# Performance work log

Hardware: AMD Instinct MI355X
Metric: run time of the kernel (lower is better)

The kernel has to match this reference:

```python
import jax, jax.numpy as jnp
import numpy as np

H = 224  # config.output_height
W = 224  # config.output_width
N = 381  # config.num_frequency_bins (one splat per bin)
B = 16   # frames rendered per batch


def setup_inputs() -> dict:
    key = jax.random.key(0)
    k1, k2, k3 = jax.random.split(key, 3)
    # positions in [-0.9, 0.9] (spiral stays inside the frame)
    positions = jax.random.uniform(k1, (B, N, 2), dtype=jnp.float32, minval=-0.9, maxval=0.9)
    colors = jax.random.uniform(k2, (B, N, 3), dtype=jnp.float32)  # RGB in [0,1]
    # sizes in pixels, matching base_size=2 + size_scale=8*softplus(...)
    sizes = jax.random.uniform(k3, (B, N), dtype=jnp.float32, minval=2.0, maxval=10.0)
    return {"positions": positions, "colors": colors, "sizes": sizes}


def reference(positions, colors, sizes):
    """Soft (differentiable) rasterization of Gaussian point splats.

    positions: [B,N,2] in [-1,1]; colors: [B,N,3] in [0,1]; sizes: [B,N] pixels.
    Returns image [B,H,W,3] in [0,1].
    """
    gy = jnp.linspace(-1.0, 1.0, H, dtype=positions.dtype)
    gx = jnp.linspace(-1.0, 1.0, W, dtype=positions.dtype)
    # squared distance from every pixel to every point: [B,N,H,W]
    dx = gx[None, None, None, :] - positions[:, :, 0, None, None]
    dy = gy[None, None, :, None] - positions[:, :, 1, None, None]
    d2 = dx * dx + dy * dy
    # pixel size -> normalized coords ([-1,1] spans H pixels)
    sigma = sizes * (2.0 / H)  # [B,N]
    inv_two_var = 1.0 / (2.0 * sigma * sigma + 1e-8)
    weights = jnp.exp(-d2 * inv_two_var[:, :, None, None])  # [B,N,H,W]
    image = jnp.einsum('bnhw,bnc->bhwc', weights, colors)   # accumulate splats
    return jnp.clip(image, 0.0, 1.0)
```

## Files before the change

### kernel.cpp

```cpp
#include <hip/hip_runtime.h>
#include <math.h>

#define HH 224
#define WW 224
#define NS 381
#define BB 16
#define TPB 256
#define TILE_W 32
#define TILE_H 32
#define TILES_X (WW / TILE_W)
#define BLKS_PER_IMG (TILES_X * (HH / TILE_H))
#define NBLK (BB * BLKS_PER_IMG)
#define NS_PAD 384
#define CUT 19.93f
#define CH 32
#define EY_STRIDE 33
#define EXT_STRIDE 40
#define MT_STRIDE 40
#define OUT_STRIDE 97

typedef _Float16 f16x8 __attribute__((ext_vector_type(8)));
typedef _Float16 f16x2 __attribute__((ext_vector_type(2)));
typedef float    f32x4 __attribute__((ext_vector_type(4)));

union SharedU {
    struct {
        float    ey[CH * EY_STRIDE];
        _Float16 ext[TILE_W * EXT_STRIDE];
        _Float16 mt[96 * MT_STRIDE];
    } s;
    float outb[TILE_W * OUT_STRIDE];
};

__global__ __launch_bounds__(TPB) void splat_render(const float* __restrict__ pos,
                                                    const float* __restrict__ col,
                                                    const float* __restrict__ siz,
                                                    float* __restrict__ out) {
    __shared__ float4 geo[NS_PAD];
    __shared__ int cnt;
    __shared__ SharedU u;

    int blk = blockIdx.x;
    int b = blk / BLKS_PER_IMG;
    int t = blk - b * BLKS_PER_IMG;
    int tile_y = t / TILES_X;
    int tile_x = t - tile_y * TILES_X;

    if (threadIdx.x == 0) cnt = 0;
    __syncthreads();

    const float gstep = 2.0f / (float)(WW - 1);
    float x0 = -1.0f + (float)(tile_x * TILE_W) * gstep;
    float x1 = x0 + (float)(TILE_W - 1) * gstep;
    float y0 = -1.0f + (float)(tile_y * TILE_H) * gstep;
    float y1 = y0 + (float)(TILE_H - 1) * gstep;

    const float2* pb = (const float2*)(pos + (size_t)b * NS * 2);
    const float*  cb = col + (size_t)b * NS * 3;
    const float*  sb = siz + (size_t)b * NS;
    int lane = threadIdx.x & 63;
    int wave = threadIdx.x >> 6;

    for (int r = 0; r < 2; ++r) {
        int i = threadIdx.x + r * TPB;
        bool pass = false;
        float4 A = make_float4(0.f, 0.f, 0.f, 0.f);
        if (i < NS) {
            float2 p = pb[i];
            float sg = sb[i] * (2.0f / (float)HH);
            float itv = 1.0f / (2.0f * sg * sg + 1e-8f);
            float ss = sqrtf(itv * 1.44269504088896340736f);
            float u_ = p.x * ss, v_ = p.y * ss;
            float dxm = fmaxf(fmaxf(x0 * ss - u_, u_ - x1 * ss), 0.0f);
            float dym = fmaxf(fmaxf(y0 * ss - v_, v_ - y1 * ss), 0.0f);
            pass = fmaf(dxm, dxm, dym * dym) < CUT;
            if (pass) {
                unsigned pr = (unsigned)fmaf(cb[3 * i + 0], 1023.0f, 0.5f);
                unsigned pg = (unsigned)fmaf(cb[3 * i + 1], 1023.0f, 0.5f);
                unsigned pc = (unsigned)fmaf(cb[3 * i + 2], 1023.0f, 0.5f);
                A = make_float4(ss, -u_, -v_, __uint_as_float(pr | (pg << 10) | (pc << 20)));
            }
        }
        unsigned long long mask = __ballot(pass);
        int ofs = __popcll(mask & ((1ull << lane) - 1ull));
        int tot = __popcll(mask);
        int base = 0;
        if (lane == 0 && tot) base = atomicAdd(&cnt, tot);
        base = __shfl(base, 0);
        if (pass) geo[base + ofs] = A;
    }
    __syncthreads();
    int m = cnt;
    int m_pad = (m + (CH - 1)) & ~(CH - 1);
    for (int i = m + threadIdx.x; i < m_pad; i += TPB)
        geo[i] = make_float4(0.f, 0.f, 0.f, 0.f);
    __syncthreads();

    int ct = wave & 1;
    int qbase = (wave >> 1) * 48;
    f32x4 acc0 = {0.f, 0.f, 0.f, 0.f};
    f32x4 acc1 = {0.f, 0.f, 0.f, 0.f};
    f32x4 acc2 = {0.f, 0.f, 0.f, 0.f};

    int p2  = threadIdx.x & 15;
    int rEy = threadIdx.x & 31;
    float gyr = y0 + (float)rEy * gstep;

    for (int nb = 0; nb < m_pad; nb += CH) {
#pragma unroll
        for (int k = 0; k < 4; ++k) {
            int n = (threadIdx.x >> 5) + 8 * k;
            float4 A = geo[nb + n];
            float dy = fmaf(gyr, A.x, A.z);
            u.s.ey[n * EY_STRIDE + rEy] = __builtin_amdgcn_exp2f(-dy * dy);
        }
        __syncthreads();
        float4 A0 = geo[nb + 2 * p2];
        float4 A1 = geo[nb + 2 * p2 + 1];
#pragma unroll
        for (int k = 0; k < 2; ++k) {
            int c = (threadIdx.x >> 4) + 16 * k;
            float gxc = x0 + (float)c * gstep;
            float dx0 = fmaf(gxc, A0.x, A0.y);
            float dx1 = fmaf(gxc, A1.x, A1.y);
            f16x2 h;
            h.x = (_Float16)__builtin_amdgcn_exp2f(-dx0 * dx0);
            h.y = (_Float16)__builtin_amdgcn_exp2f(-dx1 * dx1);
            *(f16x2*)&u.s.ext[c * EXT_STRIDE + 2 * p2] = h;
        }
        unsigned pk0 = __float_as_uint(A0.w), pk1 = __float_as_uint(A1.w);
#pragma unroll
        for (int k = 0; k < 6; ++k) {
            int q = (threadIdx.x >> 4) + 16 * k;
            int r = (q * 21846) >> 16;
            int chn = q - 3 * r;
            float cf0 = (float)((pk0 >> (10 * chn)) & 1023u) * (1.0f / 1023.0f);
            float cf1 = (float)((pk1 >> (10 * chn)) & 1023u) * (1.0f / 1023.0f);
            f16x2 h;
            h.x = (_Float16)(u.s.ey[(2 * p2) * EY_STRIDE + r] * cf0);
            h.y = (_Float16)(u.s.ey[(2 * p2 + 1) * EY_STRIDE + r] * cf1);
            *(f16x2*)&u.s.mt[q * MT_STRIDE + 2 * p2] = h;
        }
        __syncthreads();
        {
            int koff = (lane >> 4) * 8;
            f16x8 a  = *(const f16x8*)&u.s.ext[((lane & 15) + 16 * ct) * EXT_STRIDE + koff];
            f16x8 b0 = *(const f16x8*)&u.s.mt[(qbase +  0 + (lane & 15)) * MT_STRIDE + koff];
            f16x8 b1 = *(const f16x8*)&u.s.mt[(qbase + 16 + (lane & 15)) * MT_STRIDE + koff];
            f16x8 b2 = *(const f16x8*)&u.s.mt[(qbase + 32 + (lane & 15)) * MT_STRIDE + koff];
            acc0 = __builtin_amdgcn_mfma_f32_16x16x32_f16(a, b0, acc0, 0, 0, 0);
            acc1 = __builtin_amdgcn_mfma_f32_16x16x32_f16(a, b1, acc1, 0, 0, 0);
            acc2 = __builtin_amdgcn_mfma_f32_16x16x32_f16(a, b2, acc2, 0, 0, 0);
        }
        __syncthreads();
    }

    int drow = ct * 16 + (lane >> 4) * 4;
    int dcol = qbase + (lane & 15);
#pragma unroll
    for (int rr = 0; rr < 4; ++rr) {
        u.outb[(drow + rr) * OUT_STRIDE + dcol +  0] = acc0[rr];
        u.outb[(drow + rr) * OUT_STRIDE + dcol + 16] = acc1[rr];
        u.outb[(drow + rr) * OUT_STRIDE + dcol + 32] = acc2[rr];
    }
    __syncthreads();

    int tx = threadIdx.x & 7;
    int ty = threadIdx.x >> 3;
    int w0 = tile_x * TILE_W + tx * 4;
    int h  = tile_y * TILE_H + ty;
    float v[12];
#pragma unroll
    for (int j = 0; j < 4; ++j) {
        int c = tx * 4 + j;
        v[3 * j + 0] = fminf(u.outb[c * OUT_STRIDE + 3 * ty + 0], 1.f);
        v[3 * j + 1] = fminf(u.outb[c * OUT_STRIDE + 3 * ty + 1], 1.f);
        v[3 * j + 2] = fminf(u.outb[c * OUT_STRIDE + 3 * ty + 2], 1.f);
    }
    float4* o4 = (float4*)(out + ((size_t)b * (HH * WW) + (size_t)h * WW + w0) * 3);
    o4[0] = make_float4(v[0], v[1], v[2], v[3]);
    o4[1] = make_float4(v[4], v[5], v[6], v[7]);
    o4[2] = make_float4(v[8], v[9], v[10], v[11]);
}

extern "C" void kernel_launch(void* const* d_in, const int* in_sizes, int n_in,
                              void* d_out, int out_size, void* d_ws, size_t ws_size,
                              hipStream_t stream) {
    const float* pos = (const float*)d_in[0];
    const float* col = (const float*)d_in[1];
    const float* siz = (const float*)d_in[2];
    float* out = (float*)d_out;
    splat_render<<<NBLK, TPB, 0, stream>>>(pos, col, siz, out);
}
```

Baseline: 67.91 us.

## Build MFMA fragments directly in registers, removing per-chunk LDS staging and barriers

Each wave now computes its own separable Gaussian factors straight into f16 MFMA operand registers: the x-factor is multiplied by each color channel to form three A fragments, and the y-factor forms a shared B fragment. This removes the ey/ext/mt LDS staging buffers and the three __syncthreads per 32-splat chunk. Colors are stored unpacked as floats in a second LDS array instead of being 10-bit packed. The cost is redundant exp2 work across waves (each lane evaluates 16 exps per chunk) and more LDS reads of geometry and color per lane.

Result: no change. 67.25 us (-1.0%).

```diff
diff --git a/kernel.cpp b/kernel.cpp
--- a/kernel.cpp
+++ b/kernel.cpp
@@ -14,31 +14,20 @@
 #define NS_PAD 384
 #define CUT 19.93f
 #define CH 32
-#define EY_STRIDE 33
-#define EXT_STRIDE 40
-#define MT_STRIDE 40
 #define OUT_STRIDE 97
 
 typedef _Float16 f16x8 __attribute__((ext_vector_type(8)));
-typedef _Float16 f16x2 __attribute__((ext_vector_type(2)));
 typedef float    f32x4 __attribute__((ext_vector_type(4)));
 
-union SharedU {
-    struct {
-        float    ey[CH * EY_STRIDE];
-        _Float16 ext[TILE_W * EXT_STRIDE];
-        _Float16 mt[96 * MT_STRIDE];
-    } s;
-    float outb[TILE_W * OUT_STRIDE];
-};
 
 __global__ __launch_bounds__(TPB) void splat_render(const float* __restrict__ pos,
                                                     const float* __restrict__ col,
                                                     const float* __restrict__ siz,
                                                     float* __restrict__ out) {
     __shared__ float4 geo[NS_PAD];
+    __shared__ float4 colg[NS_PAD];
+    __shared__ float outb[TILE_W * OUT_STRIDE];
     __shared__ int cnt;
-    __shared__ SharedU u;
 
     int blk = blockIdx.x;
     int b = blk / BLKS_PER_IMG;
@@ -65,6 +54,7 @@
         int i = threadIdx.x + r * TPB;
         bool pass = false;
         float4 A = make_float4(0.f, 0.f, 0.f, 0.f);
+        float4 Cc = make_float4(0.f, 0.f, 0.f, 0.f);
         if (i < NS) {
             float2 p = pb[i];
             float sg = sb[i] * (2.0f / (float)HH);
@@ -75,10 +65,8 @@
             float dym = fmaxf(fmaxf(y0 * ss - v_, v_ - y1 * ss), 0.0f);
             pass = fmaf(dxm, dxm, dym * dym) < CUT;
             if (pass) {
-                unsigned pr = (unsigned)fmaf(cb[3 * i + 0], 1023.0f, 0.5f);
-                unsigned pg = (unsigned)fmaf(cb[3 * i + 1], 1023.0f, 0.5f);
-                unsigned pc = (unsigned)fmaf(cb[3 * i + 2], 1023.0f, 0.5f);
-                A = make_float4(ss, -u_, -v_, __uint_as_float(pr | (pg << 10) | (pc << 20)));
+                A = make_float4(ss, -u_, -v_, 0.f);
+                Cc = make_float4(cb[3 * i + 0], cb[3 * i + 1], cb[3 * i + 2], 0.f);
             }
         }
         unsigned long long mask = __ballot(pass);
@@ -87,81 +75,55 @@
         int base = 0;
         if (lane == 0 && tot) base = atomicAdd(&cnt, tot);
         base = __shfl(base, 0);
-        if (pass) geo[base + ofs] = A;
+        if (pass) { geo[base + ofs] = A; colg[base + ofs] = Cc; }
     }
     __syncthreads();
     int m = cnt;
     int m_pad = (m + (CH - 1)) & ~(CH - 1);
-    for (int i = m + threadIdx.x; i < m_pad; i += TPB)
-        geo[i] = make_float4(0.f, 0.f, 0.f, 0.f);
+    for (int i = m + threadIdx.x; i < m_pad; i += TPB) {
+        geo[i]  = make_float4(0.f, 0.f, 0.f, 0.f);
+        colg[i] = make_float4(0.f, 0.f, 0.f, 0.f);
+    }
     __syncthreads();
+    m_pad = __builtin_amdgcn_readfirstlane(m_pad);
 
     int ct = wave & 1;
-    int qbase = (wave >> 1) * 48;
+    int rt = wave >> 1;
+    float gxc = x0 + (float)(16 * ct + (lane & 15)) * gstep;
+    float gyr = y0 + (float)(16 * rt + (lane & 15)) * gstep;
     f32x4 acc0 = {0.f, 0.f, 0.f, 0.f};
     f32x4 acc1 = {0.f, 0.f, 0.f, 0.f};
     f32x4 acc2 = {0.f, 0.f, 0.f, 0.f};
 
-    int p2  = threadIdx.x & 15;
-    int rEy = threadIdx.x & 31;
-    float gyr = y0 + (float)rEy * gstep;
+    int kg = (lane >> 4) * 8;
 
     for (int nb = 0; nb < m_pad; nb += CH) {
+        f16x8 af0, af1, af2, bf;
 #pragma unroll
-        for (int k = 0; k < 4; ++k) {
-            int n = (threadIdx.x >> 5) + 8 * k;
-            float4 A = geo[nb + n];
+        for (int j = 0; j < 8; ++j) {
+            float4 A  = geo[nb + kg + j];
+            float4 Cc = colg[nb + kg + j];
+            float dx = fmaf(gxc, A.x, A.y);
+            float ex = __builtin_amdgcn_exp2f(-dx * dx);
             float dy = fmaf(gyr, A.x, A.z);
-            u.s.ey[n * EY_STRIDE + rEy] = __builtin_amdgcn_exp2f(-dy * dy);
+            bf[j]  = (_Float16)__builtin_amdgcn_exp2f(-dy * dy);
+            af0[j] = (_Float16)(ex * Cc.x);
+            af1[j] = (_Float16)(ex * Cc.y);
+            af2[j] = (_Float16)(ex * Cc.z);
         }
-        __syncthreads();
-        float4 A0 = geo[nb + 2 * p2];
-        float4 A1 = geo[nb + 2 * p2 + 1];
-#pragma unroll
-        for (int k = 0; k < 2; ++k) {
-            int c = (threadIdx.x >> 4) + 16 * k;
-            float gxc = x0 + (float)c * gstep;
-            float dx0 = fmaf(gxc, A0.x, A0.y);
-            float dx1 = fmaf(gxc, A1.x, A1.y);
-            f16x2 h;
-            h.x = (_Float16)__builtin_amdgcn_exp2f(-dx0 * dx0);
-            h.y = (_Float16)__builtin_amdgcn_exp2f(-dx1 * dx1);
-            *(f16x2*)&u.s.ext[c * EXT_STRIDE + 2 * p2] = h;
-        }
-        unsigned pk0 = __float_as_uint(A0.w), pk1 = __float_as_uint(A1.w);
-#pragma unroll
-        for (int k = 0; k < 6; ++k) {
-            int q = (threadIdx.x >> 4) + 16 * k;
-            int r = (q * 21846) >> 16;
-            int chn = q - 3 * r;
-            float cf0 = (float)((pk0 >> (10 * chn)) & 1023u) * (1.0f / 1023.0f);
-            float cf1 = (float)((pk1 >> (10 * chn)) & 1023u) * (1.0f / 1023.0f);
-            f16x2 h;
-            h.x = (_Float16)(u.s.ey[(2 * p2) * EY_STRIDE + r] * cf0);
-            h.y = (_Float16)(u.s.ey[(2 * p2 + 1) * EY_STRIDE + r] * cf1);
-            *(f16x2*)&u.s.mt[q * MT_STRIDE + 2 * p2] = h;
-        }
-        __syncthreads();
-        {
-            int koff = (lane >> 4) * 8;
-            f16x8 a  = *(const f16x8*)&u.s.ext[((lane & 15) + 16 * ct) * EXT_STRIDE + koff];
-            f16x8 b0 = *(const f16x8*)&u.s.mt[(qbase +  0 + (lane & 15)) * MT_STRIDE + koff];
-            f16x8 b1 = *(const f16x8*)&u.s.mt[(qbase + 16 + (lane & 15)) * MT_STRIDE + koff];
-            f16x8 b2 = *(const f16x8*)&u.s.mt[(qbase + 32 + (lane & 15)) * MT_STRIDE + koff];
-            acc0 = __builtin_amdgcn_mfma_f32_16x16x32_f16(a, b0, acc0, 0, 0, 0);
-            acc1 = __builtin_amdgcn_mfma_f32_16x16x32_f16(a, b1, acc1, 0, 0, 0);
-            acc2 = __builtin_amdgcn_mfma_f32_16x16x32_f16(a, b2, acc2, 0, 0, 0);
-        }
-        __syncthreads();
+        acc0 = __builtin_amdgcn_mfma_f32_16x16x32_f16(af0, bf, acc0, 0, 0, 0);
+        acc1 = __builtin_amdgcn_mfma_f32_16x16x32_f16(af1, bf, acc1, 0, 0, 0);
+        acc2 = __builtin_amdgcn_mfma_f32_16x16x32_f16(af2, bf, acc2, 0, 0, 0);
     }
 
-    int drow = ct * 16 + (lane >> 4) * 4;
-    int dcol = qbase + (lane & 15);
+    __syncthreads();
+    int rglob = 16 * rt + (lane & 15);
 #pragma unroll
     for (int rr = 0; rr < 4; ++rr) {
-        u.outb[(drow + rr) * OUT_STRIDE + dcol +  0] = acc0[rr];
-        u.outb[(drow + rr) * OUT_STRIDE + dcol + 16] = acc1[rr];
-        u.outb[(drow + rr) * OUT_STRIDE + dcol + 32] = acc2[rr];
+        int cglob = 16 * ct + (lane >> 4) * 4 + rr;
+        outb[cglob * OUT_STRIDE + 3 * rglob + 0] = acc0[rr];
+        outb[cglob * OUT_STRIDE + 3 * rglob + 1] = acc1[rr];
+        outb[cglob * OUT_STRIDE + 3 * rglob + 2] = acc2[rr];
     }
     __syncthreads();
 
@@ -173,9 +135,9 @@
 #pragma unroll
     for (int j = 0; j < 4; ++j) {
         int c = tx * 4 + j;
-        v[3 * j + 0] = fminf(u.outb[c * OUT_STRIDE + 3 * ty + 0], 1.f);
-        v[3 * j + 1] = fminf(u.outb[c * OUT_STRIDE + 3 * ty + 1], 1.f);
-        v[3 * j + 2] = fminf(u.outb[c * OUT_STRIDE + 3 * ty + 2], 1.f);
+        v[3 * j + 0] = fminf(outb[c * OUT_STRIDE + 3 * ty + 0], 1.f);
+        v[3 * j + 1] = fminf(outb[c * OUT_STRIDE + 3 * ty + 1], 1.f);
+        v[3 * j + 2] = fminf(outb[c * OUT_STRIDE + 3 * ty + 2], 1.f);
     }
     float4* o4 = (float4*)(out + ((size_t)b * (HH * WW) + (size_t)h * WW + w0) * 3);
     o4[0] = make_float4(v[0], v[1], v[2], v[3]);
```
